# Optimization experiments

Measured on AMD Instinct MI355X. Metric: run time of the kernel, lower is better.

## Reference

```python
import jax, jax.numpy as jnp
import numpy as np

DIM = 180; HEADS = 6; WS = 16; NUM_TOKENS = 64; RDIM = 10; CAT = 128
KS = 5; MLP_HID = 360; DTD = 64; Hh = 64; Ww = 64; B = 8; M = 64


def _ln(x, g, b, eps=1e-5):
    mu = x.mean(-1, keepdims=True)
    var = ((x - mu) ** 2).mean(-1, keepdims=True)
    return (x - mu) / jnp.sqrt(var + eps) * g + b


def _l2norm(x):
    return x / jnp.clip(jnp.linalg.norm(x, axis=-1, keepdims=True), 1e-12)


def setup_inputs() -> dict:
    key = jax.random.key(0)
    ks = jax.random.split(key, 24)
    rn = lambda k, s: jax.random.normal(k, s, jnp.float32) * 0.02
    z = lambda *s: jnp.zeros(s, jnp.float32)
    return {
        'x': jax.random.normal(ks[0], (B, Hh * Ww, DIM), jnp.float32),
        'td': jax.random.normal(ks[1], (B, M, DIM), jnp.float32),
        'norm1_g': jnp.ones((DIM,), jnp.float32), 'norm1_b': z(DIM),
        'wqkv_w': rn(ks[2], (DIM, 3 * DIM)), 'wqkv_b': z(3 * DIM),
        'atd_wq_w': rn(ks[3], (DIM, RDIM)), 'atd_wq_b': z(RDIM),
        'atd_wk_w': rn(ks[4], (DIM, RDIM)), 'atd_wk_b': z(RDIM),
        'atd_wv_w': rn(ks[5], (DIM, DIM)), 'atd_wv_b': z(DIM),
        'atd_scale': jnp.ones((1,), jnp.float32),
        'aca_proj_w': rn(ks[6], (DIM, DIM)), 'aca_proj_b': z(DIM),
        'win_rpb': rn(ks[7], ((2 * WS - 1) ** 2, HEADS)),
        'win_proj_w': rn(ks[8], (DIM, DIM)), 'win_proj_b': z(DIM),
        'fc_td_w': rn(ks[9], (DIM, DTD)), 'fc_td_b': z(DTD),
        'fc1_w': rn(ks[10], (DIM, MLP_HID)), 'fc1_b': z(MLP_HID),
        'dw_w': rn(ks[11], (MLP_HID + DTD, 1, KS, KS)), 'dw_b': z(MLP_HID + DTD),
        'fc2_w': rn(ks[12], (MLP_HID + DTD, DIM)), 'fc2_b': z(DIM),
        'norm2_g': jnp.ones((DIM,), jnp.float32), 'norm2_b': z(DIM),
        'rpi_sa': jax.random.randint(ks[13], (WS * WS, WS * WS), 0, (2 * WS - 1) ** 2),
        'h': Hh, 'w': Ww,
    }


def reference(x, td, norm1_g, norm1_b, wqkv_w, wqkv_b, atd_wq_w, atd_wq_b,
              atd_wk_w, atd_wk_b, atd_wv_w, atd_wv_b, atd_scale,
              aca_proj_w, aca_proj_b, win_rpb, win_proj_w, win_proj_b,
              fc_td_w, fc_td_b, fc1_w, fc1_b, dw_w, dw_b, fc2_w, fc2_b,
              norm2_g, norm2_b, rpi_sa, h, w):
    b, n, c = x.shape
    hd = c // HEADS
    shortcut = x
    xn = _ln(x, norm1_g, norm1_b)
    qkv = xn @ wqkv_w + wqkv_b  # [b, n, 3c]

    # --- ATD_CA: l2-normalized cross-attention to token dictionary ---
    q = xn @ atd_wq_w + atd_wq_b          # [b, n, rd]
    kk = td @ atd_wk_w + atd_wk_b         # [b, m, rd]
    vv = td @ atd_wv_w + atd_wv_b         # [b, m, c]
    logit_scale = 1.0 + jnp.clip(atd_scale, 0.0, 3.0) * np.log(NUM_TOKENS)
    sim = jnp.einsum('bnr,bmr->bnm', _l2norm(q), _l2norm(kk)) * logit_scale
    attn_atd = jax.nn.softmax(sim, axis=-1)
    x_atd = jnp.einsum('bnm,bmc->bnc', attn_atd, vv)
    tk_id = jnp.argmax(attn_atd, axis=-1)  # [b, n]

    # --- AC_MSA: category-sorted grouped attention ---
    gs = min(n, CAT); ng = (n + gs - 1) // gs; pad_n = ng * gs - n
    sort_idx = jnp.argsort(tk_id, axis=-1)
    inv_idx = jnp.argsort(sort_idx, axis=-1)  # inverse permutation
    sq = jnp.take_along_axis(qkv, sort_idx[:, :, None], axis=1)
    sq = jnp.concatenate([sq, jnp.flip(sq[:, n - pad_n:n, :], axis=1)], axis=1)
    g = sq.reshape(b, ng, gs, 3, HEADS, hd).transpose(3, 0, 1, 4, 2, 5)
    qa, ka, va = g[0], g[1], g[2]          # [b, ng, H, gs, hd]
    a = jax.nn.softmax(jnp.einsum('bgHid,bgHjd->bgHij', qa, ka) * hd ** -0.5, axis=-1)
    y = jnp.einsum('bgHij,bgHjd->bgHid', a, va).transpose(0, 1, 3, 2, 4)
    y = y.reshape(b, n + pad_n, c)[:, :n]
    x_aca = jnp.take_along_axis(y, inv_idx[:, :, None], axis=1) @ aca_proj_w + aca_proj_b

    # --- gather per-token dictionary features for FFN ---
    td_proj = td @ fc_td_w + fc_td_b       # [b, m, dtd]
    x_td = jnp.take_along_axis(td_proj, jnp.broadcast_to(tk_id[:, :, None], (b, n, DTD)), axis=1)

    # --- window attention (shift_size = 0, no mask) ---
    nwh, nww = h // WS, w // WS
    win = qkv.reshape(b, nwh, WS, nww, WS, 3 * c).transpose(0, 1, 3, 2, 4, 5)
    win = win.reshape(-1, WS * WS, 3 * c)
    B_ = win.shape[0]; N = WS * WS
    wq = win.reshape(B_, N, 3, HEADS, hd).transpose(2, 0, 3, 1, 4)
    qw, kw, vw = wq[0] * hd ** -0.5, wq[1], wq[2]
    bias = win_rpb[rpi_sa.reshape(-1)].reshape(N, N, HEADS).transpose(2, 0, 1)[None]
    aw = jax.nn.softmax(jnp.einsum('wHid,wHjd->wHij', qw, kw) + bias, axis=-1)
    ow = jnp.einsum('wHij,wHjd->wHid', aw, vw).transpose(0, 2, 1, 3).reshape(B_, N, c)
    ow = ow @ win_proj_w + win_proj_b
    attn_x = ow.reshape(b, nwh, nww, WS, WS, c).transpose(0, 1, 3, 2, 4, 5).reshape(b, n, c)

    x = shortcut + x_atd + attn_x + x_aca

    # --- ConvFFN_td with depthwise conv branch ---
    x2 = _ln(x, norm2_g, norm2_b)
    h1 = jax.nn.gelu(x2 @ fc1_w + fc1_b, approximate=False)
    hc = jnp.concatenate([h1, x_td], axis=-1)  # [b, n, C]
    C = hc.shape[-1]
    img = jnp.swapaxes(hc, 1, 2).reshape(b, C, h, w)
    conv = jax.lax.conv_general_dilated(img, dw_w, (1, 1), 'SAME',
        dimension_numbers=('NCHW', 'OIHW', 'NCHW'), feature_group_count=C)
    conv = jax.nn.gelu(conv + dw_b[None, :, None, None], approximate=False)
    hc = hc + jnp.swapaxes(conv.reshape(b, C, n), 1, 2)
    return x + hc @ fc2_w + fc2_b
```

## Files before the change

### kernel.cpp

```cpp
#include <hip/hip_runtime.h>
#include <hip/hip_bf16.h>
#include <math.h>

#define BB      8
#define NTOK    4096
#define CDIM    180
#define C3      540
#define NHEADS  6
#define HD      30
#define MDICT   64
#define RD      10
#define DTD     64
#define MHID    360
#define CCAT    424
#define WS      16
#define WIN_N   256
#define GS      128
#define NG      32
#define ROWS    (BB*NTOK)
#define KP1     192
#define KP2     448
#define QKVP    576

typedef __hip_bfloat16 bf16;
typedef short v8s __attribute__((ext_vector_type(8)));
typedef float f32x4 __attribute__((ext_vector_type(4)));
typedef unsigned int u32x4 __attribute__((ext_vector_type(4)));

__device__ __forceinline__ float gelu_exact(float x) {
    return 0.5f * x * (1.0f + erff(x * 0.70710678118654752f));
}
__device__ __forceinline__ float wave_sum(float v) {
    #pragma unroll
    for (int off = 32; off > 0; off >>= 1) v += __shfl_xor(v, off, 64);
    return v;
}
__device__ __forceinline__ unsigned short f2b(float v) {
    unsigned u = __float_as_uint(v);
    return (unsigned short)((u + 0x7FFFu + ((u >> 16) & 1u)) >> 16);
}
__device__ __forceinline__ float b2f(unsigned short h) {
    return __uint_as_float(((unsigned)h) << 16);
}
__device__ __forceinline__ unsigned packbf(float lo, float hi) {
    return (unsigned)f2b(lo) | ((unsigned)f2b(hi) << 16);
}
__device__ __forceinline__ void gload16(const void* g, void* l) {
    __builtin_amdgcn_global_load_lds(
        (const __attribute__((address_space(1))) void*)g,
        (__attribute__((address_space(3))) void*)l, 16, 0, 0);
}

__global__ __launch_bounds__(256) void detect_kernel(const void* __restrict__ x,
                                                     int* __restrict__ flag,
                                                     int* __restrict__ diag)
{
    __shared__ int cnt;
    if (threadIdx.x == 0) { cnt = 0; *diag = 0; }
    __syncthreads();
    const unsigned short* u = (const unsigned short*)x;
    int c = 0;
    for (int i = threadIdx.x; i < 2048; i += 256) {
        unsigned short e = u[2 * i] & 0x7F80;
        if (e >= 0x4300) c++;
    }
    atomicAdd(&cnt, c);
    __syncthreads();
    if (threadIdx.x == 0) *flag = (cnt > 16) ? 1 : 0;
}

#define NCVT 23
struct CvtArgs {
    const void* src[NCVT];
    float* dst[NCVT];
    int cum[NCVT + 1];
};
__global__ __launch_bounds__(256) void convert_all_kernel(CvtArgs a, int total,
        const int* __restrict__ flag)
{
    int i = blockIdx.x * 256 + threadIdx.x;
    if (i >= total) return;
    int s = 0;
    while (i >= a.cum[s + 1]) s++;
    int off = i - a.cum[s];
    if (*flag) a.dst[s][off] = ((const float*)a.src[s])[off];
    else       a.dst[s][off] = __bfloat162float(((const bf16*)a.src[s])[off]);
}

__global__ __launch_bounds__(256) void check_f32_kernel(const float* __restrict__ buf,
        int n, int bit, int* __restrict__ diag)
{
    int i = blockIdx.x * 256 + threadIdx.x;
    if (i >= n) return;
    unsigned u = __float_as_uint(buf[i]);
    if ((u & 0x7F800000u) == 0x7F800000u) atomicOr(diag, bit);
}

__global__ __launch_bounds__(256) void emit_kernel(const float* __restrict__ src,
        void* __restrict__ out, const int* __restrict__ flag,
        const int* __restrict__ diag, int n)
{
    int i = blockIdx.x * 256 + threadIdx.x;
    if (i >= n) return;
    float v = src[i];
    int d = *diag;
    if (d) v = 100.f + 32.f * (float)d;
    if (*flag) ((float*)out)[i] = v;
    else       ((bf16*)out)[i]  = __float2bfloat16(v);
}

__global__ __launch_bounds__(256) void zero_tail_kernel(bf16* __restrict__ buf)
{
    int idx = blockIdx.x * 256 + threadIdx.x;
    int row = idx / 12, c = idx % 12;
    buf[(size_t)row * KP1 + CDIM + c] = __float2bfloat16(0.f);
}

__global__ __launch_bounds__(256) void zero_qkvpad_kernel(bf16* __restrict__ qb)
{
    int idx = blockIdx.x * 256 + threadIdx.x;
    int row = idx / 36, r = idx % 36;
    int sec = r / 12, rr = r % 12, hh = rr >> 1, d = 30 + (rr & 1);
    qb[(size_t)row * QKVP + sec * 192 + hh * 32 + d] = __float2bfloat16(0.f);
}

__global__ __launch_bounds__(256) void packW_kernel(const void* __restrict__ W,
        bf16* __restrict__ Wt, int K, int N, int Kpad, int total,
        const int* __restrict__ flag)
{
    int idx = blockIdx.x * 256 + threadIdx.x;
    if (idx >= total) return;
    int n = idx / Kpad, k = idx % Kpad;
    float v = 0.f;
    if (k < K && n < N) {
        size_t src = (size_t)k * N + n;
        v = (*flag) ? ((const float*)W)[src]
                    : __bfloat162float(((const bf16*)W)[src]);
    }
    Wt[idx] = __float2bfloat16(v);
}

__global__ __launch_bounds__(256) void packWT_kernel(const float* __restrict__ w,
        float* __restrict__ wT)
{
    int idx = blockIdx.x * 256 + threadIdx.x;
    if (idx >= 25 * KP2) return;
    int kk = idx / KP2, ch = idx % KP2;
    wT[idx] = (ch < CCAT) ? w[ch * 25 + kk] : 0.f;
}

__global__ __launch_bounds__(256) void bias_pre_kernel(const int* __restrict__ rpi,
        const float* __restrict__ rpb, float* __restrict__ bias_t)
{
    int idx = blockIdx.x * 256 + threadIdx.x;
    int h = idx >> 16, ij = idx & 65535;
    bias_t[idx] = rpb[rpi[ij] * NHEADS + h];
}

template<bool GELU_, bool ADDRES, bool BIAS_, int OM>
__global__ __launch_bounds__(256) void mgemm_kernel(
        const bf16* __restrict__ A, int lda,
        const bf16* __restrict__ Wt, int ldw,
        const float* __restrict__ bias,
        const float* __restrict__ res, int ldr,
        float* __restrict__ outF, int ldo, int N, int K)
{
    __shared__ __align__(16) unsigned short As[128][32];
    __shared__ __align__(16) unsigned short Bs[64][32];
    int tid = threadIdx.x;
    int wave = tid >> 6, lane = tid & 63;
    int quad = lane >> 4, mr = lane & 15;
    int row0 = blockIdx.y * 128, col0 = blockIdx.x * 64;
    int ar = tid >> 2, ac = (tid & 3) * 8;
    f32x4 z = {0.f, 0.f, 0.f, 0.f};
    f32x4 acc[2][4] = {{z, z, z, z}, {z, z, z, z}};
    const unsigned short* Au = (const unsigned short*)A;
    const unsigned short* Wu = (const unsigned short*)Wt;
    for (int k0 = 0; k0 < K; k0 += 32) {
        gload16(&Au[(size_t)(row0 + ar) * lda + k0 + ac],      &As[ar][ac]);
        gload16(&Au[(size_t)(row0 + 64 + ar) * lda + k0 + ac], &As[64 + ar][ac]);
        gload16(&Wu[(size_t)(col0 + ar) * ldw + k0 + ac],      &Bs[ar][ac]);
        __syncthreads();
        v8s bfr[4];
        #pragma unroll
        for (int ni = 0; ni < 4; ni++)
            bfr[ni] = *(const v8s*)&Bs[ni * 16 + mr][quad * 8];
        #pragma unroll
        for (int s = 0; s < 2; s++) {
            v8s a = *(const v8s*)&As[wave * 32 + s * 16 + mr][quad * 8];
            #pragma unroll
            for (int ni = 0; ni < 4; ni++)
                acc[s][ni] = __builtin_amdgcn_mfma_f32_16x16x32_bf16(
                    a, bfr[ni], acc[s][ni], 0, 0, 0);
        }
        __syncthreads();
    }
    if (OM == 1) {
        bf16* outb = (bf16*)outF;
        #pragma unroll
        for (int ni = 0; ni < 4; ni++) {
            int gc = col0 + ni * 16 + mr;
            if (gc >= N) continue;
            float bv = bias[gc];
            int sec = gc / 180, rem = gc - sec * 180;
            int hh = rem / 30, d = rem - hh * 30;
            int slot = sec * 192 + hh * 32 + d;
            float sc = (sec == 0) ? 0.18257418583505536f : 1.f;
            #pragma unroll
            for (int s = 0; s < 2; s++) {
                #pragma unroll
                for (int r = 0; r < 4; r++) {
                    int gr = row0 + wave * 32 + s * 16 + quad * 4 + r;
                    outb[(size_t)gr * QKVP + slot] =
                        __float2bfloat16((acc[s][ni][r] + bv) * sc);
                }
            }
        }
        return;
    }
    #pragma unroll
    for (int ni = 0; ni < 4; ni++) {
        int gc = col0 + ni * 16 + mr;
        if (gc >= N) continue;
        float bv = BIAS_ ? bias[gc] : 0.f;
        #pragma unroll
        for (int s = 0; s < 2; s++) {
            #pragma unroll
            for (int r = 0; r < 4; r++) {
                int gr = row0 + wave * 32 + s * 16 + quad * 4 + r;
                float v = acc[s][ni][r] + bv;
                if (GELU_) v = gelu_exact(v);
                if (ADDRES) v += res[(size_t)gr * ldr + gc];
                outF[(size_t)gr * ldo + gc] = v;
            }
        }
    }
}

__global__ __launch_bounds__(256) void av_mgemm_kernel(
        const bf16* __restrict__ P, const bf16* __restrict__ vvT,
        const float* __restrict__ xres, float* __restrict__ accout)
{
    __shared__ unsigned short As[64][32];
    __shared__ unsigned short Bs[64][32];
    int tid = threadIdx.x;
    int wave = tid >> 6, lane = tid & 63;
    int quad = lane >> 4, mr = lane & 15;
    int row0 = blockIdx.y * 64, col0 = blockIdx.x * 64;
    int bz = blockIdx.z;
    const unsigned short* Au = (const unsigned short*)P + (size_t)bz * NTOK * MDICT;
    const unsigned short* Wu = (const unsigned short*)vvT + (size_t)bz * 192 * MDICT;
    const float* res = xres + (size_t)bz * NTOK * CDIM;
    float* outF = accout + (size_t)bz * NTOK * CDIM;
    f32x4 z = {0.f, 0.f, 0.f, 0.f};
    f32x4 acc[4] = {z, z, z, z};
    for (int k0 = 0; k0 < MDICT; k0 += 32) {
        #pragma unroll
        for (int e = 0; e < 8; e++) {
            int idx = tid * 8 + e;
            int r = idx >> 5, c = idx & 31;
            As[r][c] = Au[(size_t)(row0 + r) * MDICT + k0 + c];
            Bs[r][c] = Wu[(size_t)(col0 + r) * MDICT + k0 + c];
        }
        __syncthreads();
        v8s a;
        #pragma unroll
        for (int j = 0; j < 8; j++) a[j] = (short)As[wave * 16 + mr][quad * 8 + j];
        #pragma unroll
        for (int ni = 0; ni < 4; ni++) {
            v8s b;
            #pragma unroll
            for (int j = 0; j < 8; j++) b[j] = (short)Bs[ni * 16 + mr][quad * 8 + j];
            acc[ni] = __builtin_amdgcn_mfma_f32_16x16x32_bf16(a, b, acc[ni], 0, 0, 0);
        }
        __syncthreads();
    }
    #pragma unroll
    for (int ni = 0; ni < 4; ni++) {
        int gc = col0 + ni * 16 + mr;
        if (gc >= CDIM) continue;
        #pragma unroll
        for (int r = 0; r < 4; r++) {
            int gr = row0 + wave * 16 + quad * 4 + r;
            float v = acc[ni][r] + res[(size_t)gr * CDIM + gc];
            outF[(size_t)gr * CDIM + gc] = v;
        }
    }
}

__global__ __launch_bounds__(256, 4) void win_mfma_kernel(const bf16* __restrict__ qkvb,
        const float* __restrict__ bias_t, bf16* __restrict__ outb)
{
    int b = blockIdx.y;
    int widx = blockIdx.x / NHEADS;
    int hh = blockIdx.x % NHEADS;
    int wy = widx >> 2, wx = widx & 3;
    int tid = threadIdx.x;
    int wave = tid >> 6, lane = tid & 63, quad = lane >> 4, mr = lane & 15;
    __shared__ __align__(16) unsigned short Ks[64][40];
    __shared__ __align__(16) unsigned short Vt[32][80];

    size_t brow = (size_t)b * NTOK;
    const unsigned short* qu = (const unsigned short*)qkvb;

    v8s aq[4];
    #pragma unroll
    for (int tt = 0; tt < 4; tt++) {
        int m = (wave * 4 + tt) * 16 + mr;
        int nt_ = (wy * WS + (m >> 4)) * 64 + wx * WS + (m & 15);
        aq[tt] = *(const v8s*)&qu[(brow + nt_) * QKVP + hh * 32 + quad * 8];
    }
    f32x4 z = {0.f, 0.f, 0.f, 0.f};
    f32x4 oacc[4][2] = {{z, z}, {z, z}, {z, z}, {z, z}};
    float m_r[4], l_r[4];
    #pragma unroll
    for (int tt = 0; tt < 4; tt++) { m_r[tt] = -3.0e38f; l_r[tt] = 0.f; }
    const float* btab = bias_t + (size_t)hh * WIN_N * WIN_N;

    for (int kc = 0; kc < WIN_N; kc += 64) {
        {
            int j = tid >> 2, dg = (tid & 3) * 8;
            int tok = kc + j;
            int nt_ = (wy * WS + (tok >> 4)) * 64 + wx * WS + (tok & 15);
            const unsigned short* base = qu + (brow + nt_) * QKVP + hh * 32;
            v8s kv = *(const v8s*)&base[192 + dg];
            v8s vv = *(const v8s*)&base[384 + dg];
            *(v8s*)&Ks[j][dg] = kv;
            #pragma unroll
            for (int jj = 0; jj < 8; jj++)
                Vt[dg + jj][j] = (unsigned short)vv[jj];
        }
        __syncthreads();
        #pragma unroll
        for (int tt = 0; tt < 4; tt++) {
            f32x4 s[4];
            #pragma unroll
            for (int nt = 0; nt < 4; nt++) {
                v8s bk = *(const v8s*)&Ks[nt * 16 + mr][quad * 8];
                s[nt] = __builtin_amdgcn_mfma_f32_16x16x32_bf16(bk, aq[tt], z, 0, 0, 0);
            }
            int qg = (wave * 4 + tt) * 16 + mr;
            const float* bi = btab + (size_t)qg * WIN_N + kc;
            float mc = -3.0e38f;
            #pragma unroll
            for (int nt = 0; nt < 4; nt++) {
                f32x4 b4 = *(const f32x4*)(bi + nt * 16 + quad * 4);
                s[nt][0] += b4[0]; s[nt][1] += b4[1];
                s[nt][2] += b4[2]; s[nt][3] += b4[3];
                mc = fmaxf(mc, fmaxf(fmaxf(s[nt][0], s[nt][1]),
                                     fmaxf(s[nt][2], s[nt][3])));
            }
            mc = fmaxf(mc, __shfl_xor(mc, 16, 64));
            mc = fmaxf(mc, __shfl_xor(mc, 32, 64));
            float mn = fmaxf(m_r[tt], mc);
            float alpha = __expf(m_r[tt] - mn);
            m_r[tt] = mn;
            float ls = 0.f;
            #pragma unroll
            for (int nt = 0; nt < 4; nt++) {
                #pragma unroll
                for (int r = 0; r < 4; r++) {
                    float pp = __expf(s[nt][r] - mn);
                    ls += pp;
                    s[nt][r] = pp;
                }
            }
            ls += __shfl_xor(ls, 16, 64);
            ls += __shfl_xor(ls, 32, 64);
            l_r[tt] = l_r[tt] * alpha + ls;
            unsigned dpk[4][2];
            #pragma unroll
            for (int nt = 0; nt < 4; nt++) {
                dpk[nt][0] = packbf(s[nt][0], s[nt][1]);
                dpk[nt][1] = packbf(s[nt][2], s[nt][3]);
            }
            #pragma unroll
            for (int r = 0; r < 4; r++) {
                float av = __shfl(alpha, quad * 4 + r, 64);
                oacc[tt][0][r] *= av;
                oacc[tt][1][r] *= av;
            }
            #pragma unroll
            for (int c = 0; c < 2; c++) {
                union { u32x4 u; v8s s8; } afu;
                #pragma unroll
                for (int t = 0; t < 4; t++) {
                    int srcl = (((quad * 2 + (t >> 1)) & 3) << 4) | mr;
                    unsigned r0 = (unsigned)__shfl((int)dpk[2 * c][t & 1], srcl, 64);
                    unsigned r1 = (unsigned)__shfl((int)dpk[2 * c + 1][t & 1], srcl, 64);
                    afu.u[t] = (quad & 2) ? r1 : r0;
                }
                #pragma unroll
                for (int dt = 0; dt < 2; dt++) {
                    v8s bv = *(const v8s*)&Vt[dt * 16 + mr][c * 32 + quad * 8];
                    oacc[tt][dt] = __builtin_amdgcn_mfma_f32_16x16x32_bf16(
                        afu.s8, bv, oacc[tt][dt], 0, 0, 0);
                }
            }
        }
        __syncthreads();
    }
    #pragma unroll
    for (int tt = 0; tt < 4; tt++) {
        float il = 1.f / l_r[tt];
        #pragma unroll
        for (int r = 0; r < 4; r++) {
            float ilr = __shfl(il, quad * 4 + r, 64);
            int m = (wave * 4 + tt) * 16 + quad * 4 + r;
            int nt_ = (wy * WS + (m >> 4)) * 64 + wx * WS + (m & 15);
            #pragma unroll
            for (int dt = 0; dt < 2; dt++) {
                int d = dt * 16 + mr;
                if (d >= HD) continue;
                outb[(brow + nt_) * KP1 + hh * HD + d] =
                    __float2bfloat16(oacc[tt][dt][r] * ilr);
            }
        }
    }
}

__global__ __launch_bounds__(256, 4) void acmsa_mfma_kernel(const bf16* __restrict__ qkvb,
        const int* __restrict__ sidx, bf16* __restrict__ outb)
{
    int b = blockIdx.y;
    int g = blockIdx.x / NHEADS;
    int hh = blockIdx.x % NHEADS;
    int tid = threadIdx.x;
    int wave = tid >> 6, lane = tid & 63, quad = lane >> 4, mr = lane & 15;
    __shared__ int toks[GS];
    __shared__ __align__(16) unsigned short Ks[64][40];
    __shared__ __align__(16) unsigned short Vt[32][80];

    size_t brow = (size_t)b * NTOK;
    if (tid < GS) toks[tid] = sidx[brow + (size_t)g * GS + tid];
    __syncthreads();
    const unsigned short* qu = (const unsigned short*)qkvb;

    v8s aq[2];
    #pragma unroll
    for (int tt = 0; tt < 2; tt++) {
        int m = (wave * 2 + tt) * 16 + mr;
        aq[tt] = *(const v8s*)&qu[(brow + toks[m]) * QKVP + hh * 32 + quad * 8];
    }
    f32x4 z = {0.f, 0.f, 0.f, 0.f};
    f32x4 oacc[2][2] = {{z, z}, {z, z}};
    float m_r[2], l_r[2];
    #pragma unroll
    for (int tt = 0; tt < 2; tt++) { m_r[tt] = -3.0e38f; l_r[tt] = 0.f; }

    for (int kc = 0; kc < GS; kc += 64) {
        {
            int j = tid >> 2, dg = (tid & 3) * 8;
            int tok = toks[kc + j];
            const unsigned short* base = qu + (brow + tok) * QKVP + hh * 32;
            v8s kv = *(const v8s*)&base[192 + dg];
            v8s vv = *(const v8s*)&base[384 + dg];
            *(v8s*)&Ks[j][dg] = kv;
            #pragma unroll
            for (int jj = 0; jj < 8; jj++)
                Vt[dg + jj][j] = (unsigned short)vv[jj];
        }
        __syncthreads();
        #pragma unroll
        for (int tt = 0; tt < 2; tt++) {
            f32x4 s[4];
            #pragma unroll
            for (int nt = 0; nt < 4; nt++) {
                v8s bk = *(const v8s*)&Ks[nt * 16 + mr][quad * 8];
                s[nt] = __builtin_amdgcn_mfma_f32_16x16x32_bf16(bk, aq[tt], z, 0, 0, 0);
            }
            float mc = -3.0e38f;
            #pragma unroll
            for (int nt = 0; nt < 4; nt++)
                mc = fmaxf(mc, fmaxf(fmaxf(s[nt][0], s[nt][1]),
                                     fmaxf(s[nt][2], s[nt][3])));
            mc = fmaxf(mc, __shfl_xor(mc, 16, 64));
            mc = fmaxf(mc, __shfl_xor(mc, 32, 64));
            float mn = fmaxf(m_r[tt], mc);
            float alpha = __expf(m_r[tt] - mn);
            m_r[tt] = mn;
            float ls = 0.f;
            #pragma unroll
            for (int nt = 0; nt < 4; nt++) {
                #pragma unroll
                for (int r = 0; r < 4; r++) {
                    float pp = __expf(s[nt][r] - mn);
                    ls += pp;
                    s[nt][r] = pp;
                }
            }
            ls += __shfl_xor(ls, 16, 64);
            ls += __shfl_xor(ls, 32, 64);
            l_r[tt] = l_r[tt] * alpha + ls;
            unsigned dpk[4][2];
            #pragma unroll
            for (int nt = 0; nt < 4; nt++) {
                dpk[nt][0] = packbf(s[nt][0], s[nt][1]);
                dpk[nt][1] = packbf(s[nt][2], s[nt][3]);
            }
            #pragma unroll
            for (int r = 0; r < 4; r++) {
                float av = __shfl(alpha, quad * 4 + r, 64);
                oacc[tt][0][r] *= av;
                oacc[tt][1][r] *= av;
            }
            #pragma unroll
            for (int c = 0; c < 2; c++) {
                union { u32x4 u; v8s s8; } afu;
                #pragma unroll
                for (int t = 0; t < 4; t++) {
                    int srcl = (((quad * 2 + (t >> 1)) & 3) << 4) | mr;
                    unsigned r0 = (unsigned)__shfl((int)dpk[2 * c][t & 1], srcl, 64);
                    unsigned r1 = (unsigned)__shfl((int)dpk[2 * c + 1][t & 1], srcl, 64);
                    afu.u[t] = (quad & 2) ? r1 : r0;
                }
                #pragma unroll
                for (int dt = 0; dt < 2; dt++) {
                    v8s bv = *(const v8s*)&Vt[dt * 16 + mr][c * 32 + quad * 8];
                    oacc[tt][dt] = __builtin_amdgcn_mfma_f32_16x16x32_bf16(
                        afu.s8, bv, oacc[tt][dt], 0, 0, 0);
                }
            }
        }
        __syncthreads();
    }
    #pragma unroll
    for (int tt = 0; tt < 2; tt++) {
        float il = 1.f / l_r[tt];
        #pragma unroll
        for (int r = 0; r < 4; r++) {
            float ilr = __shfl(il, quad * 4 + r, 64);
            int m = (wave * 2 + tt) * 16 + quad * 4 + r;
            int tok = toks[m];
            #pragma unroll
            for (int dt = 0; dt < 2; dt++) {
                int d = dt * 16 + mr;
                if (d >= HD) continue;
                outb[(brow + tok) * KP1 + hh * HD + d] =
                    __float2bfloat16(oacc[tt][dt][r] * ilr);
            }
        }
    }
}

__global__ __launch_bounds__(64) void ln_kernel(const float* __restrict__ x,
        const float* __restrict__ g, const float* __restrict__ be,
        float* __restrict__ out, bf16* __restrict__ outb)
{
    int row = blockIdx.x; int t = threadIdx.x;
    const float* xr = x + (size_t)row * CDIM;
    float v0 = xr[t];
    float v1 = xr[t + 64];
    float v2 = (t < CDIM - 128) ? xr[t + 128] : 0.f;
    float s1 = wave_sum(v0 + v1 + v2);
    float s2 = wave_sum(v0*v0 + v1*v1 + v2*v2);
    float mu = s1 / (float)CDIM;
    float var = s2 / (float)CDIM - mu * mu;
    float rs = rsqrtf(var + 1e-5f);
    float o0 = (v0 - mu) * rs * g[t]      + be[t];
    float o1 = (v1 - mu) * rs * g[t + 64] + be[t + 64];
    float o2 = (t < CDIM - 128) ? ((v2 - mu) * rs * g[t + 128] + be[t + 128]) : 0.f;
    float* o = out + (size_t)row * CDIM;
    o[t] = o0; o[t + 64] = o1;
    if (t < CDIM - 128) o[t + 128] = o2;
    bf16* ob = outb + (size_t)row * KP1;
    ob[t]       = __float2bfloat16(o0);
    ob[t + 64]  = __float2bfloat16(o1);
    ob[t + 128] = __float2bfloat16(o2);
}

__global__ __launch_bounds__(64) void td_pre_kernel(const float* __restrict__ td,
        const float* __restrict__ wk, const float* __restrict__ wkb,
        const float* __restrict__ wv, const float* __restrict__ wvb,
        const float* __restrict__ wtd, const float* __restrict__ wtdb,
        float* __restrict__ kkn, bf16* __restrict__ vvT, float* __restrict__ tdp)
{
    int blk = blockIdx.x;
    int b = blk >> 6, m = blk & 63;
    int t = threadIdx.x;
    __shared__ float tr[CDIM];
    __shared__ float sk[RD];
    __shared__ float snorm;
    const float* tdr = td + (size_t)blk * CDIM;
    tr[t] = tdr[t]; tr[t + 64] = tdr[t + 64];
    if (t < CDIM - 128) tr[t + 128] = tdr[t + 128];
    __syncthreads();
    if (t < RD) {
        float s = wkb[t];
        for (int k = 0; k < CDIM; k++) s += tr[k] * wk[k * RD + t];
        sk[t] = s;
    }
    __syncthreads();
    if (t == 0) {
        float s = 0.f;
        #pragma unroll
        for (int j = 0; j < RD; j++) s += sk[j] * sk[j];
        snorm = fmaxf(sqrtf(s), 1e-12f);
    }
    __syncthreads();
    if (t < RD) kkn[(size_t)blk * RD + t] = sk[t] / snorm;
    for (int c = t; c < 192; c += 64) {
        float s = 0.f;
        if (c < CDIM) {
            s = wvb[c];
            for (int k = 0; k < CDIM; k++) s += tr[k] * wv[k * CDIM + c];
        }
        vvT[((size_t)(b * 192 + c)) * MDICT + m] = __float2bfloat16(s);
    }
    {
        float s = wtdb[t];
        for (int k = 0; k < CDIM; k++) s += tr[k] * wtd[k * DTD + t];
        tdp[(size_t)blk * DTD + t] = s;
    }
}

__global__ __launch_bounds__(64) void atd_soft_kernel(const float* __restrict__ xn,
        const float* __restrict__ wq, const float* __restrict__ wqb,
        const float* __restrict__ scale_p, const float* __restrict__ kkn,
        bf16* __restrict__ Pout, int* __restrict__ tk_id)
{
    int row = blockIdx.x;
    int b = row >> 12;
    int t = threadIdx.x;
    const float* xrow = xn + (size_t)row * CDIM;
    float v0 = xrow[t];
    float v1 = xrow[t + 64];
    float v2 = (t < CDIM - 128) ? xrow[t + 128] : 0.f;
    float sq[RD];
    #pragma unroll
    for (int j = 0; j < RD; j++) {
        float part = v0 * wq[t * RD + j] + v1 * wq[(t + 64) * RD + j];
        if (t < CDIM - 128) part += v2 * wq[(t + 128) * RD + j];
        sq[j] = wave_sum(part) + wqb[j];
    }
    float qn = 0.f;
    #pragma unroll
    for (int j = 0; j < RD; j++) qn += sq[j] * sq[j];
    qn = fmaxf(sqrtf(qn), 1e-12f);
    float ls = 1.0f + fminf(fmaxf(scale_p[0], 0.f), 3.f) * 4.158883083359672f;
    const float* kr = kkn + ((size_t)b * MDICT + t) * RD;
    float s = 0.f;
    #pragma unroll
    for (int j = 0; j < RD; j++) s += sq[j] * kr[j];
    s = s / qn * ls;
    float mv = s; int mi = t;
    #pragma unroll
    for (int off = 32; off > 0; off >>= 1) {
        float ov = __shfl_xor(mv, off, 64);
        int   oi = __shfl_xor(mi, off, 64);
        if (ov > mv || (ov == mv && oi < mi)) { mv = ov; mi = oi; }
    }
    float e = __expf(s - mv);
    float denom = wave_sum(e);
    Pout[(size_t)row * MDICT + t] = __float2bfloat16(e / denom);
    if (t == 0) tk_id[row] = mi;
}

__global__ __launch_bounds__(256) void sort_kernel(const int* __restrict__ tk_id,
                                                   int* __restrict__ sidx)
{
    int b = blockIdx.x; int tid = threadIdx.x;
    __shared__ int keys[NTOK];
    __shared__ int cnt[256];
    __shared__ int off[256];
    const int* kb = tk_id + (size_t)b * NTOK;
    for (int i = tid; i < NTOK; i += 256) keys[i] = kb[i];
    __syncthreads();
    int v = tid >> 2, seg = tid & 3;
    int lo = seg * 1024, hi = lo + 1024;
    int c = 0;
    for (int i = lo; i < hi; i++) c += (keys[i] == v);
    cnt[tid] = c;
    __syncthreads();
    if (tid == 0) {
        int run = 0;
        for (int l = 0; l < 256; l++) { off[l] = run; run += cnt[l]; }
    }
    __syncthreads();
    int o = off[tid];
    int* sb = sidx + (size_t)b * NTOK;
    for (int i = lo; i < hi; i++) if (keys[i] == v) sb[o++] = i;
}

__global__ __launch_bounds__(256) void gather_td_kernel(const int* __restrict__ tk_id,
        const float* __restrict__ tdp, float* __restrict__ hc)
{
    int idx = blockIdx.x * 256 + threadIdx.x;
    int row = idx >> 6, j = idx & 63;
    int b = row >> 12;
    int tk = tk_id[row];
    hc[(size_t)row * CCAT + MHID + j] = tdp[((size_t)b * MDICT + tk) * DTD + j];
}

#define CHK3 64
#define CTW  8
#define CTH  8
#define CHW  12
#define CHP  144
#define CSPX 68
__global__ __launch_bounds__(256) void conv_kernel(const float* __restrict__ hc,
        const float* __restrict__ wT, const float* __restrict__ wb,
        bf16* __restrict__ outb)
{
    int ch0 = blockIdx.x * CHK3;
    int tile = blockIdx.y;
    int b = blockIdx.z;
    int ty0 = (tile >> 3) * CTH, tx0 = (tile & 7) * CTW;
    __shared__ __align__(16) float sh[CHP][CSPX];
    int tid = threadIdx.x;
    for (int idx = tid; idx < CHP * CHK3; idx += 256) {
        int pix = idx >> 6, ch = idx & 63;
        int gy = ty0 + pix / CHW - 2, gx = tx0 + pix % CHW - 2;
        int chg = ch0 + ch;
        float v = 0.f;
        if (gy >= 0 && gy < 64 && gx >= 0 && gx < 64 && chg < CCAT)
            v = hc[((size_t)b * NTOK + gy * 64 + gx) * CCAT + chg];
        sh[pix][ch] = v;
    }
    __syncthreads();
    int q = tid & 3, p = tid >> 2;
    int px = p & 7, py = p >> 3;
    int cb = q * 16;
    int pc = py * CHW + px;
    v8s pk0, pk1;
    #pragma unroll
    for (int sub = 0; sub < 4; sub++) {
        int cs = cb + sub * 4;
        const float* wtc = wT + ch0 + cs;
        f32x4 acc = {0.f, 0.f, 0.f, 0.f};
        #pragma unroll
        for (int dy = 0; dy < 5; dy++) {
            #pragma unroll
            for (int dx = 0; dx < 5; dx++) {
                f32x4 sv = *(const f32x4*)&sh[pc + dy * CHW + dx][cs];
                f32x4 wv = *(const f32x4*)&wtc[(dy * 5 + dx) * KP2];
                acc += sv * wv;
            }
            __builtin_amdgcn_sched_barrier(0);
        }
        f32x4 ctr = *(const f32x4*)&sh[pc + 2 * CHW + 2][cs];
        #pragma unroll
        for (int c = 0; c < 4; c++) {
            int chg = ch0 + cs + c;
            float v = 0.f;
            if (chg < CCAT) {
                float gv = gelu_exact(acc[c] + wb[chg]);
                v = ctr[c] + gv;
            }
            int lc = sub * 4 + c;
            if (lc < 8) pk0[lc] = (short)f2b(v);
            else        pk1[lc - 8] = (short)f2b(v);
        }
        __builtin_amdgcn_sched_barrier(0);
    }
    size_t obase = ((size_t)b * NTOK + (ty0 + py) * 64 + tx0 + px) * KP2 + ch0 + cb;
    unsigned short* ob = (unsigned short*)outb + obase;
    *(v8s*)ob = pk0;
    *(v8s*)(ob + 8) = pk1;
}

extern "C" void kernel_launch(void* const* d_in, const int* in_sizes, int n_in,
                              void* d_out, int out_size, void* d_ws, size_t ws_size,
                              hipStream_t stream)
{
    (void)n_in; (void)ws_size; (void)out_size;
    const int* rpi = (const int*)d_in[28];

    float* p = (float*)d_ws;
    float* xn    = p; p += (size_t)ROWS * CDIM;
    float* acc   = p; p += (size_t)ROWS * CDIM;
    float* tmp1  = p; p += (size_t)ROWS * CDIM;
    float* qkv   = p; p += (size_t)ROWS * C3;
    float* hcnew = p; p += (size_t)ROWS * CCAT;
    float* kkn   = p; p += (size_t)BB * MDICT * RD;
    bf16*  vvT   = (bf16*)p; p += (size_t)BB * 192 * MDICT / 2;
    float* tdp   = p; p += (size_t)BB * MDICT * DTD;
    int*   tk_id = (int*)p; p += ROWS;
    int*   sidx  = (int*)p; p += ROWS;
    int*   flag  = (int*)p; p += 64;
    int*   diag  = (int*)p; p += 64;
    bf16* wtqkv = (bf16*)p; p += 576 * KP1 / 2;
    bf16* wtaca = (bf16*)p; p += 192 * KP1 / 2;
    bf16* wtwin = (bf16*)p; p += 192 * KP1 / 2;
    bf16* wtfc1 = (bf16*)p; p += 384 * KP1 / 2;
    bf16* wtfc2 = (bf16*)p; p += 192 * KP2 / 2;
    float* cin[28];
    for (int i = 0; i < 28; i++) { cin[i] = p; p += in_sizes[i]; }
    float* bias_t = p; p += (size_t)NHEADS * WIN_N * WIN_N;
    float* wT     = p; p += 25 * KP2;

    float* hc      = qkv;
    bf16*  qkvb    = (bf16*)qkv;
    bf16*  xnb     = (bf16*)hcnew;
    bf16*  tmp1b   = (bf16*)(hcnew + (size_t)ROWS * KP1 / 2);
    bf16*  hcnewb2 = (bf16*)hcnew;
    bf16*  Pbuf    = (bf16*)tmp1;

    detect_kernel<<<1, 256, 0, stream>>>(d_in[0], flag, diag);
    {
        CvtArgs ca;
        int total = 0, s = 0;
        for (int i = 0; i < 28; i++) {
            if (i == 4 || i == 13 || i == 16 || i == 20 || i == 24) continue;
            ca.src[s] = d_in[i];
            ca.dst[s] = cin[i];
            ca.cum[s] = total;
            total += in_sizes[i];
            s++;
        }
        ca.cum[s] = total;
        convert_all_kernel<<<(total + 255) / 256, 256, 0, stream>>>(ca, total, flag);
    }
    const float *x = cin[0], *td = cin[1], *n1g = cin[2], *n1b = cin[3],
        *wqkv_b = cin[5], *wq_w = cin[6], *wq_b = cin[7],
        *wk_w = cin[8], *wk_b = cin[9], *wv_w = cin[10], *wv_b = cin[11],
        *atd_scale = cin[12], *aca_b = cin[14], *win_rpb = cin[15],
        *winp_b = cin[17], *fctd_w = cin[18], *fctd_b = cin[19],
        *fc1_b = cin[21], *dw_w = cin[22], *dw_b = cin[23], *fc2_b = cin[25],
        *n2g = cin[26], *n2b = cin[27];

    packW_kernel<<<576 * KP1 / 256, 256, 0, stream>>>(d_in[4],  wtqkv, CDIM, C3,   KP1, 576 * KP1, flag);
    packW_kernel<<<192 * KP1 / 256, 256, 0, stream>>>(d_in[13], wtaca, CDIM, CDIM, KP1, 192 * KP1, flag);
    packW_kernel<<<192 * KP1 / 256, 256, 0, stream>>>(d_in[16], wtwin, CDIM, CDIM, KP1, 192 * KP1, flag);
    packW_kernel<<<384 * KP1 / 256, 256, 0, stream>>>(d_in[20], wtfc1, CDIM, MHID, KP1, 384 * KP1, flag);
    packW_kernel<<<192 * KP2 / 256, 256, 0, stream>>>(d_in[24], wtfc2, CCAT, CDIM, KP2, 192 * KP2, flag);
    bias_pre_kernel<<<NHEADS * WIN_N * WIN_N / 256, 256, 0, stream>>>(rpi, win_rpb, bias_t);
    packWT_kernel<<<(25 * KP2 + 255) / 256, 256, 0, stream>>>(dw_w, wT);

    td_pre_kernel<<<BB * MDICT, 64, 0, stream>>>(td, wk_w, wk_b, wv_w, wv_b,
                                                 fctd_w, fctd_b, kkn, vvT, tdp);
    ln_kernel<<<ROWS, 64, 0, stream>>>(x, n1g, n1b, xn, xnb);
    mgemm_kernel<false, false, true, 1><<<dim3(9, ROWS / 128), 256, 0, stream>>>(
        xnb, KP1, wtqkv, KP1, wqkv_b, nullptr, 0, (float*)qkvb, QKVP, C3, KP1);
    zero_qkvpad_kernel<<<ROWS * 36 / 256, 256, 0, stream>>>(qkvb);
    atd_soft_kernel<<<ROWS, 64, 0, stream>>>(xn, wq_w, wq_b, atd_scale, kkn, Pbuf, tk_id);
    av_mgemm_kernel<<<dim3(3, NTOK / 64, BB), 256, 0, stream>>>(Pbuf, vvT, x, acc);
    sort_kernel<<<BB, 256, 0, stream>>>(tk_id, sidx);
    zero_tail_kernel<<<ROWS * 12 / 256, 256, 0, stream>>>(tmp1b);
    acmsa_mfma_kernel<<<dim3(NG * NHEADS, BB), 256, 0, stream>>>(qkvb, sidx, tmp1b);
    mgemm_kernel<false, true, true, 0><<<dim3(3, ROWS / 128), 256, 0, stream>>>(
        tmp1b, KP1, wtaca, KP1, aca_b, acc, CDIM, acc, CDIM, CDIM, KP1);
    win_mfma_kernel<<<dim3(16 * NHEADS, BB), 256, 0, stream>>>(qkvb, bias_t, tmp1b);
    mgemm_kernel<false, true, true, 0><<<dim3(3, ROWS / 128), 256, 0, stream>>>(
        tmp1b, KP1, wtwin, KP1, winp_b, acc, CDIM, acc, CDIM, CDIM, KP1);
    ln_kernel<<<ROWS, 64, 0, stream>>>(acc, n2g, n2b, xn, xnb);
    mgemm_kernel<true, false, true, 0><<<dim3(6, ROWS / 128), 256, 0, stream>>>(
        xnb, KP1, wtfc1, KP1, fc1_b, nullptr, 0, hc, CCAT, MHID, KP1);
    gather_td_kernel<<<ROWS * 64 / 256, 256, 0, stream>>>(tk_id, tdp, hc);
    conv_kernel<<<dim3(7, 64, BB), 256, 0, stream>>>(hc, wT, dw_b, hcnewb2);
    mgemm_kernel<false, true, true, 0><<<dim3(3, ROWS / 128), 256, 0, stream>>>(
        hcnewb2, KP2, wtfc2, KP2, fc2_b, acc, CDIM, tmp1, CDIM, CDIM, KP2);
    check_f32_kernel<<<(ROWS * CDIM + 255) / 256, 256, 0, stream>>>(tmp1, ROWS * CDIM, 8, diag);
    emit_kernel<<<(ROWS * CDIM + 255) / 256, 256, 0, stream>>>(
        tmp1, d_out, flag, diag, ROWS * CDIM);
}
```

Before: 753.5 us.

## Restructure depthwise conv for register row reuse and shared-memory weights

The depthwise 5x5 conv kernel now has each thread compute 4 adjacent pixels for 4 channels. Each thread loads 8 input vectors per kernel row and reuses them across the 5 horizontal taps, instead of reloading per tap. Conv weights are staged into shared memory in-kernel straight from the original layout, which removes the separate packWT transpose kernel and its global scratch buffer. The input tile load is vectorized to float4. The cost is more registers per thread, narrower 8-byte output stores instead of 16-byte ones, and every block redoing the weight transpose.

```diff
diff --git a/kernel.cpp b/kernel.cpp
--- a/kernel.cpp
+++ b/kernel.cpp
@@ -24,6 +24,7 @@
 
 typedef __hip_bfloat16 bf16;
 typedef short v8s __attribute__((ext_vector_type(8)));
+typedef short v4s __attribute__((ext_vector_type(4)));
 typedef float f32x4 __attribute__((ext_vector_type(4)));
 typedef unsigned int u32x4 __attribute__((ext_vector_type(4)));
 
@@ -138,15 +139,6 @@
                     : __bfloat162float(((const bf16*)W)[src]);
     }
     Wt[idx] = __float2bfloat16(v);
-}
-
-__global__ __launch_bounds__(256) void packWT_kernel(const float* __restrict__ w,
-        float* __restrict__ wT)
-{
-    int idx = blockIdx.x * 256 + threadIdx.x;
-    if (idx >= 25 * KP2) return;
-    int kk = idx / KP2, ch = idx % KP2;
-    wT[idx] = (ch < CCAT) ? w[ch * 25 + kk] : 0.f;
 }
 
 __global__ __launch_bounds__(256) void bias_pre_kernel(const int* __restrict__ rpi,
@@ -699,7 +691,7 @@
 #define CHP  144
 #define CSPX 68
 __global__ __launch_bounds__(256) void conv_kernel(const float* __restrict__ hc,
-        const float* __restrict__ wT, const float* __restrict__ wb,
+        const float* __restrict__ w, const float* __restrict__ wb,
         bf16* __restrict__ outb)
 {
     int ch0 = blockIdx.x * CHK3;
@@ -707,56 +699,63 @@
     int b = blockIdx.z;
     int ty0 = (tile >> 3) * CTH, tx0 = (tile & 7) * CTW;
     __shared__ __align__(16) float sh[CHP][CSPX];
+    __shared__ __align__(16) float wt[25][CHK3];
     int tid = threadIdx.x;
-    for (int idx = tid; idx < CHP * CHK3; idx += 256) {
-        int pix = idx >> 6, ch = idx & 63;
+    for (int idx = tid; idx < CHP * 16; idx += 256) {
+        int pix = idx >> 4, cq = idx & 15;
         int gy = ty0 + pix / CHW - 2, gx = tx0 + pix % CHW - 2;
+        int chg = ch0 + cq * 4;
+        f32x4 v = {0.f, 0.f, 0.f, 0.f};
+        if (gy >= 0 && gy < 64 && gx >= 0 && gx < 64 && chg < CCAT)
+            v = *(const f32x4*)&hc[((size_t)b * NTOK + gy * 64 + gx) * CCAT + chg];
+        *(f32x4*)&sh[pix][cq * 4] = v;
+    }
+    for (int idx = tid; idx < 25 * CHK3; idx += 256) {
+        int kk = idx >> 6, ch = idx & 63;
         int chg = ch0 + ch;
-        float v = 0.f;
-        if (gy >= 0 && gy < 64 && gx >= 0 && gx < 64 && chg < CCAT)
-            v = hc[((size_t)b * NTOK + gy * 64 + gx) * CCAT + chg];
-        sh[pix][ch] = v;
-    }
-    __syncthreads();
-    int q = tid & 3, p = tid >> 2;
-    int px = p & 7, py = p >> 3;
-    int cb = q * 16;
-    int pc = py * CHW + px;
-    v8s pk0, pk1;
-    #pragma unroll
-    for (int sub = 0; sub < 4; sub++) {
-        int cs = cb + sub * 4;
-        const float* wtc = wT + ch0 + cs;
-        f32x4 acc = {0.f, 0.f, 0.f, 0.f};
-        #pragma unroll
-        for (int dy = 0; dy < 5; dy++) {
-            #pragma unroll
-            for (int dx = 0; dx < 5; dx++) {
-                f32x4 sv = *(const f32x4*)&sh[pc + dy * CHW + dx][cs];
-                f32x4 wv = *(const f32x4*)&wtc[(dy * 5 + dx) * KP2];
-                acc += sv * wv;
-            }
-            __builtin_amdgcn_sched_barrier(0);
-        }
-        f32x4 ctr = *(const f32x4*)&sh[pc + 2 * CHW + 2][cs];
+        wt[kk][ch] = (chg < CCAT) ? w[chg * 25 + kk] : 0.f;
+    }
+    __syncthreads();
+    int q = tid & 15, pg = tid >> 4;
+    int py = pg >> 1, px0 = (pg & 1) * 4;
+    int cs = q * 4;
+    f32x4 z4 = {0.f, 0.f, 0.f, 0.f};
+    f32x4 acc[4] = {z4, z4, z4, z4};
+    #pragma unroll
+    for (int dy = 0; dy < 5; dy++) {
+        const float* srow = &sh[(py + dy) * CHW + px0][cs];
+        f32x4 r[8];
+        #pragma unroll
+        for (int j = 0; j < 8; j++)
+            r[j] = *(const f32x4*)(srow + j * CSPX);
+        #pragma unroll
+        for (int kx = 0; kx < 5; kx++) {
+            f32x4 wv = *(const f32x4*)&wt[dy * 5 + kx][cs];
+            acc[0] += r[kx] * wv;
+            acc[1] += r[kx + 1] * wv;
+            acc[2] += r[kx + 2] * wv;
+            acc[3] += r[kx + 3] * wv;
+        }
+        __builtin_amdgcn_sched_barrier(0);
+    }
+    #pragma unroll
+    for (int px = 0; px < 4; px++) {
+        f32x4 ctr = *(const f32x4*)&sh[(py + 2) * CHW + px0 + px + 2][cs];
+        v4s pk;
         #pragma unroll
         for (int c = 0; c < 4; c++) {
             int chg = ch0 + cs + c;
             float v = 0.f;
             if (chg < CCAT) {
-                float gv = gelu_exact(acc[c] + wb[chg]);
+                float gv = gelu_exact(acc[px][c] + wb[chg]);
                 v = ctr[c] + gv;
             }
-            int lc = sub * 4 + c;
-            if (lc < 8) pk0[lc] = (short)f2b(v);
-            else        pk1[lc - 8] = (short)f2b(v);
-        }
-        __builtin_amdgcn_sched_barrier(0);
-    }
-    size_t obase = ((size_t)b * NTOK + (ty0 + py) * 64 + tx0 + px) * KP2 + ch0 + cb;
-    unsigned short* ob = (unsigned short*)outb + obase;
-    *(v8s*)ob = pk0;
-    *(v8s*)(ob + 8) = pk1;
+            pk[c] = (short)f2b(v);
+        }
+        size_t obase = ((size_t)b * NTOK + (ty0 + py) * 64 + tx0 + px0 + px) * KP2
+                       + ch0 + cs;
+        *(v4s*)((unsigned short*)outb + obase) = pk;
+    }
 }
 
 extern "C" void kernel_launch(void* const* d_in, const int* in_sizes, int n_in,
@@ -787,7 +786,6 @@
     float* cin[28];
     for (int i = 0; i < 28; i++) { cin[i] = p; p += in_sizes[i]; }
     float* bias_t = p; p += (size_t)NHEADS * WIN_N * WIN_N;
-    float* wT     = p; p += 25 * KP2;
 
     float* hc      = qkv;
     bf16*  qkvb    = (bf16*)qkv;
@@ -825,7 +823,6 @@
     packW_kernel<<<384 * KP1 / 256, 256, 0, stream>>>(d_in[20], wtfc1, CDIM, MHID, KP1, 384 * KP1, flag);
     packW_kernel<<<192 * KP2 / 256, 256, 0, stream>>>(d_in[24], wtfc2, CCAT, CDIM, KP2, 192 * KP2, flag);
     bias_pre_kernel<<<NHEADS * WIN_N * WIN_N / 256, 256, 0, stream>>>(rpi, win_rpb, bias_t);
-    packWT_kernel<<<(25 * KP2 + 255) / 256, 256, 0, stream>>>(dw_w, wT);
 
     td_pre_kernel<<<BB * MDICT, 64, 0, stream>>>(td, wk_w, wk_b, wv_w, wv_b,
                                                  fctd_w, fctd_b, kkn, vvT, tdp);
@@ -847,7 +844,7 @@
     mgemm_kernel<true, false, true, 0><<<dim3(6, ROWS / 128), 256, 0, stream>>>(
         xnb, KP1, wtfc1, KP1, fc1_b, nullptr, 0, hc, CCAT, MHID, KP1);
     gather_td_kernel<<<ROWS * 64 / 256, 256, 0, stream>>>(tk_id, tdp, hc);
-    conv_kernel<<<dim3(7, 64, BB), 256, 0, stream>>>(hc, wT, dw_b, hcnewb2);
+    conv_kernel<<<dim3(7, 64, BB), 256, 0, stream>>>(hc, dw_w, dw_b, hcnewb2);
     mgemm_kernel<false, true, true, 0><<<dim3(3, ROWS / 128), 256, 0, stream>>>(
         hcnewb2, KP2, wtfc2, KP2, fc2_b, acc, CDIM, tmp1, CDIM, CDIM, KP2);
     check_f32_kernel<<<(ROWS * CDIM + 255) / 256, 256, 0, stream>>>(tmp1, ROWS * CDIM, 8, diag);
```

Measured after the change: 721.1 us. -4.3%, faster.
